# Kernel tuning notes

Measured on AMD Instinct MI355X. Metric: run time of the kernel, lower is better.

The kernel has to match this reference:

```python
import jax, jax.numpy as jnp
import numpy as np

# ---- fixed constants from stft2hcfp.__init__ ----
FS = 16000.0; FR = 2.0; FC = 27.5; TC = 1.0 / 4487.0; NPO = 48
N = int(FS / FR)                      # 8000 FFT length
HALF_N = int(round(N / 2))            # 4000
SQRT_N = float(np.sqrt(N))
HIGH_FREQ_IDX = int(round(1.0 / TC / FR) + 1)   # 2245
HIGH_QUEF_IDX = int(round(FS / FC)) + 1         # 583
CUT_Q = int(round(FS * TC))           # 4  (cepstrum cutoff)
TOTAL_BINS = 4 * 88                   # 352 log-freq bins
NUM_HARMONIC = 5

def _central_freqs():
    stop = 1.0 / TC
    nest = int(np.ceil(np.log2(stop / FC)) * NPO)
    cf = []
    for i in range(nest):
        c = FC * 2.0 ** (float(i) / NPO)
        if c < stop:
            cf.append(c)
        else:
            break
    return cf

CF = _central_freqs()   # 353 central frequencies
NEST = len(CF)

def _freq_matrix():
    # triangular log-frequency filterbank over linear freq axis
    f = (FS * np.linspace(0, 0.5, HALF_N, endpoint=True))[:HIGH_FREQ_IDX]
    W = np.zeros((NEST - 1, len(f)), np.float32)
    for i in range(1, NEST - 1):
        l = int(round(CF[i - 1] / FR)); r = int(round(CF[i + 1] / FR) + 1)
        if l >= r - 1:
            W[i, l] = 1.0
        else:
            for j in range(l, r):
                if CF[i - 1] < f[j] < CF[i]:
                    W[i, j] = (f[j] - CF[i - 1]) / (CF[i] - CF[i - 1])
                elif CF[i] < f[j] < CF[i + 1]:
                    W[i, j] = (CF[i + 1] - f[j]) / (CF[i + 1] - CF[i])
    return W

def _quef_matrix():
    q = np.arange(HIGH_QUEF_IDX) / FS + 1e-6
    fq = 1.0 / q
    W = np.zeros((NEST - 1, len(fq)), np.float32)
    for i in range(1, NEST - 1):
        for j in range(int(round(FS / CF[i + 1])), int(round(FS / CF[i - 1]) + 1)):
            if j >= len(fq):
                continue
            if CF[i - 1] < fq[j] < CF[i]:
                W[i, j] = (fq[j] - CF[i - 1]) / (CF[i] - CF[i - 1])
            elif CF[i] < fq[j] < CF[i + 1]:
                W[i, j] = (CF[i + 1] - fq[j]) / (CF[i + 1] - CF[i])
    return W

# harmonic shift indices: closest central freq to (k+1)*27.5 Hz, k=0..5
HIDS = [int(np.argmin(np.abs(np.asarray(CF) - (k + 1) * FC))) for k in range(NUM_HARMONIC + 1)]


def _nonlinear(x, g, cutoff):
    # relu + pow(g), then zero first/last `cutoff` rows along axis 1.
    # safe pow: grad is 0 where x<=0 (matches relu-masked torch behavior, no inf at 0)
    y = jnp.where(x > 0, jnp.where(x > 0, x, 1.0) ** g, 0.0)
    y = y.at[:, :cutoff].set(0.0).at[:, -cutoff:].set(0.0)
    return y


def setup_inputs() -> dict:
    key = jax.random.key(0)
    dx = jax.random.uniform(key, (8, 512, N), dtype=jnp.float32)  # [B, T, 8000] spectrogram
    return {
        "dx": dx,
        "W_freq": jnp.asarray(_freq_matrix()),   # [352, 2245]
        "W_quef": jnp.asarray(_quef_matrix()),   # [352, 583]
    }


def reference(dx, W_freq, W_quef):
    tfr0 = jnp.swapaxes(dx, 1, 2)                       # [B, F=8000, T]
    # CFP layer 1: real part of FFT over freq axis -> cepstrum, nonlinear g=0.6
    ceps = jnp.fft.fft(tfr0, axis=1).real / SQRT_N      # [B, 8000, T]
    ceps = _nonlinear(ceps, 0.6, CUT_Q)
    # log-frequency mappings (banded triangular filterbanks)
    tfr0h = tfr0[:, :HIGH_FREQ_IDX]                      # [B, 2245, T]
    cepsh = ceps[:, :HIGH_QUEF_IDX]                      # [B, 583, T]
    tfrL0 = jnp.einsum('kf,bft->bkt', W_freq, tfr0h)     # [B, 352, T]
    tfrLQ = jnp.einsum('kq,bqt->bkt', W_quef, cepsh)     # [B, 352, T]
    # harmonic stacking: shift down (spectral) / shift up (cepstral)
    har_s = [jnp.pad(tfrL0[:, h:TOTAL_BINS], ((0, 0), (0, h), (0, 0))) for h in HIDS]
    har_c = [jnp.pad(tfrLQ[:, :TOTAL_BINS - h], ((0, 0), (h, 0), (0, 0))) for h in HIDS]
    piece = jnp.concatenate([jnp.stack(har_s, axis=1), jnp.stack(har_c, axis=1)], axis=1)
    return jnp.swapaxes(piece, 2, 3)                     # [B, 12, T, 352]
```

## Files before the change

kernel.cpp:

```cpp
#include <hip/hip_runtime.h>
#include <hip/hip_bf16.h>
#include <limits.h>

typedef __attribute__((ext_vector_type(8))) short short8;
typedef __attribute__((ext_vector_type(4))) float f32x4;
typedef __attribute__((ext_vector_type(16))) float f32x16;

#define NN 8000
#define NCOL 4096
#define KBINS 352
#define QPAD 640
#define QH 160
#define BN 128
#define KC 4
#define NTILE 64
#define KSTEP 16
#define CUTQ 4
#define T_ 512
#define WFB 64
#define WQB 20

#define GLL16(g, l) __builtin_amdgcn_global_load_lds( \
    (const __attribute__((address_space(1))) unsigned int*)(g), \
    (__attribute__((address_space(3))) unsigned int*)(l), 16, 0, 0)

static __device__ __forceinline__ ushort bfc(float f){
  __hip_bfloat16 h = __float2bfloat16(f);
  return *reinterpret_cast<ushort*>(&h);
}
static __device__ __forceinline__ float b2f(ushort u){
  unsigned v = ((unsigned)u) << 16; float f; __builtin_memcpy(&f, &v, 4); return f;
}

__global__ void gen_cos_k(ushort* __restrict__ cosg, int HQI){
  int n = blockIdx.x*256 + threadIdx.x;
  int q = blockIdx.y;
  float v = 0.f;
  if (q < HQI){
    int m = (q*n) % NN;
    v = cosf((float)m * 7.8539816339744831e-4f);
  }
  int kt = n >> 6, s8 = (n >> 3) & 7, e = n & 7;
  cosg[(size_t)kt*(QPAD*64) + (size_t)q*64 + (((s8 ^ (q & 7)) << 3) | e)] = bfc(v);
}

#define PADI(j) ((j) + ((j) >> 5))
__global__ __launch_bounds__(512) void fold_k(const float* __restrict__ dx,
                                              ushort* __restrict__ xf){
  __shared__ float sbuf[4232];
  int row = blockIdx.x;
  int t = threadIdx.x;
  const float* rp = dx + (size_t)row*NN;
  {
    int j0 = t*8;
    f32x4 v0 = *(const f32x4*)(rp + 3896 + j0);
    f32x4 v1 = *(const f32x4*)(rp + 3896 + j0 + 4);
    #pragma unroll
    for (int e=0;e<4;e++) sbuf[PADI(j0+e)] = v0[e];
    #pragma unroll
    for (int e=0;e<4;e++) sbuf[PADI(j0+4+e)] = v1[e];
    if (t == 0){
      #pragma unroll
      for (int e=0;e<8;e++) sbuf[PADI(4096+e)] = rp[7992+e];
    }
  }
  __syncthreads();

  int n0 = t*8;
  f32x4 p0 = *(const f32x4*)(rp + n0);
  f32x4 p1 = *(const f32x4*)(rp + n0 + 4);
  float pr[8] = {p0[0],p0[1],p0[2],p0[3],p1[0],p1[1],p1[2],p1[3]};
  short8 o;
  #pragma unroll
  for (int e=0;e<8;e++){
    int n = n0 + e;
    float v;
    if (n == 0)          v = pr[0];
    else if (n < 4000)   v = pr[e] + sbuf[PADI(4104 - n)];
    else if (n == 4000)  v = pr[e];
    else                 v = 0.f;
    o[e] = (short)bfc(v);
  }
  int kt = n0 >> 6, s8 = (n0 >> 3) & 7;
  *(short8*)(&xf[((size_t)kt*NCOL + row)*64 + ((s8 ^ (row & 7)) << 3)]) = o;
}

__global__ void bp_k(const float* __restrict__ Wf, const float* __restrict__ Wq,
                     int HFI, int HQI, int* __restrict__ fLo, int* __restrict__ qLo,
                     float* __restrict__ WfT, float* __restrict__ WqT){
  __shared__ int slo, shi;
  int r = blockIdx.x;
  bool isF = (blockIdx.y == 0);
  const float* W = isF ? Wf : Wq;
  int width = isF ? HFI : HQI;
  int bw    = isF ? WFB : WQB;
  float* WT = isF ? WfT : WqT;
  int* Lo   = isF ? fLo : qLo;
  if (threadIdx.x==0){ slo = INT_MAX; shi = -1; }
  __syncthreads();
  int mylo = INT_MAX, myhi = -1;
  for (int c = threadIdx.x; c < width; c += 256){
    if (W[(size_t)r*width + c] != 0.f){ if (c < mylo) mylo = c; if (c > myhi) myhi = c; }
  }
  atomicMin(&slo, mylo); atomicMax(&shi, myhi);
  __syncthreads();
  int l = (shi < 0) ? 0 : slo, h = (shi < 0) ? 0 : shi + 1;
  if (threadIdx.x==0) Lo[r] = l;
  for (int j = threadIdx.x; j < bw; j += 256){
    float v = 0.f;
    if (l + j < h) v = W[(size_t)r*width + l + j];
    WT[(size_t)j*KBINS + r] = v;
  }
}

__global__ __launch_bounds__(256, 2) void gemm_k(const ushort* __restrict__ xf,
                                                 const ushort* __restrict__ cosg,
                                                 ushort* __restrict__ part){
  __shared__ ushort As[2][QH*64];
  __shared__ ushort Bs[2][BN*64];
  int tid = threadIdx.x;
  int nb = blockIdx.x, qh = blockIdx.y, kc = blockIdx.z;
  int lane = tid & 63, wn = tid >> 6;
  int l31 = lane & 31, lh = lane >> 5;
  int kt0 = kc*KSTEP, ktE = kt0 + KSTEP;

  const ushort* ag0 = cosg + (size_t)qh*(QH*64) + tid*8;
  const ushort* bg0 = xf + (size_t)nb*(BN*64) + tid*8;

  #define STAGE(kt_, buf_) { \
    const ushort* ag_ = ag0 + (size_t)(kt_)*(QPAD*64); \
    _Pragma("unroll") \
    for (int i_=0;i_<5;i_++) GLL16(ag_ + i_*2048, &As[buf_][tid*8 + i_*2048]); \
    const ushort* bg_ = bg0 + (size_t)(kt_)*(NCOL*64); \
    _Pragma("unroll") \
    for (int i_=0;i_<4;i_++) GLL16(bg_ + i_*2048, &Bs[buf_][tid*8 + i_*2048]); }

  f32x16 acc[5];
  #pragma unroll
  for (int a=0;a<5;a++) acc[a] = (f32x16)0.f;

  STAGE(kt0, 0);

  int cur = 0;
  for (int kt = kt0; kt < ktE; ++kt){
    bool stg = (kt + 1 < ktE);
    if (stg){
      STAGE(kt+1, cur^1);
      asm volatile("s_waitcnt vmcnt(9)" ::: "memory");
    } else {
      asm volatile("s_waitcnt vmcnt(0)" ::: "memory");
    }
    __builtin_amdgcn_s_barrier();
    __builtin_amdgcn_sched_barrier(0);
    const ushort* Ac = &As[cur][0];
    const ushort* Bc = &Bs[cur][0];
    #pragma unroll
    for (int p=0;p<4;p++){
      int brow = wn*32 + l31;
      short8 dfr = *(const short8*)(Bc + brow*64 + ((((p<<1)|lh) ^ (brow & 7)) << 3));
      short8 cfr[5];
      #pragma unroll
      for (int a=0;a<5;a++){
        int arow = a*32 + l31;
        cfr[a] = *(const short8*)(Ac + arow*64 + ((((p<<1)|lh) ^ (arow & 7)) << 3));
      }
      __builtin_amdgcn_s_setprio(1);
      #pragma unroll
      for (int a=0;a<5;a++)
        acc[a] = __builtin_amdgcn_mfma_f32_32x32x16_bf16(dfr, cfr[a], acc[a], 0,0,0);
      __builtin_amdgcn_s_setprio(0);
    }
    __builtin_amdgcn_sched_barrier(0);
    __builtin_amdgcn_s_barrier();
    __builtin_amdgcn_sched_barrier(0);
    cur ^= 1;
  }

  ushort* pb = part + (size_t)kc*NCOL*QPAD;
  #pragma unroll
  for (int a=0;a<5;a++){
    int q = qh*QH + a*32 + l31;
    int colb = nb*BN + wn*32 + 4*lh;
    #pragma unroll
    for (int r=0;r<16;r++){
      int col = colb + (r&3) + 8*(r>>2);
      pb[(size_t)col*QPAD + q] = bfc(acc[a][r]);
    }
  }
}

__global__ __launch_bounds__(384) void fuse_k(const float* __restrict__ dx,
        const ushort* __restrict__ part,
        const float* __restrict__ WfT, const float* __restrict__ WqT,
        const int* __restrict__ fLo, const int* __restrict__ qLo,
        float* __restrict__ out, int HFI, int HQI){
  __shared__ float xr[2368];
  __shared__ float yq[QPAD];
  __shared__ float tl0[KBINS];
  __shared__ float tlq[KBINS];
  int col = blockIdx.x;
  int b = col >> 9, t = col & 511;
  int tid = threadIdx.x;
  const float invs = 0.011180339887498949f;

  for (int f = tid; f < 2368; f += 384) xr[f] = (f < HFI) ? dx[(size_t)col*NN + f] : 0.f;
  const ushort* pc = part + (size_t)col*QPAD;
  for (int q = tid; q < QPAD; q += 384){
    float y = 0.f;
    if (q < HQI){
      float s = 0.f;
      #pragma unroll
      for (int kc=0; kc<KC; kc++) s += b2f(pc[(size_t)kc*NCOL*QPAD + q]);
      s *= invs;
      if (q >= CUTQ && s > 0.f) y = powf(s, 0.6f);
    }
    yq[q] = y;
  }
  __syncthreads();

  if (tid < KBINS){
    int k = tid;
    int lo = fLo[k];
    float aF = 0.f;
    #pragma unroll
    for (int j=0;j<WFB;j++) aF += WfT[j*KBINS + k] * xr[lo + j];
    int ql = qLo[k];
    float aQ = 0.f;
    #pragma unroll
    for (int j=0;j<WQB;j++) aQ += WqT[j*KBINS + k] * yq[ql + j];
    tl0[k] = aF; tlq[k] = aQ;
  }
  __syncthreads();

  const int hids[6] = {0,48,76,96,111,124};
  for (int u = tid; u < 12*KBINS; u += 384){
    int j = u / KBINS;
    int k = u - j*KBINS;
    int h = hids[(j < 6) ? j : j - 6];
    float v;
    if (j < 6) v = (k + h < KBINS) ? tl0[k + h] : 0.f;
    else       v = (k >= h)        ? tlq[k - h] : 0.f;
    out[(((size_t)b*12 + j)*T_ + t)*KBINS + k] = v;
  }
}

extern "C" void kernel_launch(void* const* d_in, const int* in_sizes, int n_in,
                              void* d_out, int out_size, void* d_ws, size_t ws_size,
                              hipStream_t stream){
  const float* dx = (const float*)d_in[0];
  const float* Wf = (const float*)d_in[1];
  const float* Wq = (const float*)d_in[2];
  int HFI = in_sizes[1] / KBINS;
  int HQI = in_sizes[2] / KBINS;
  float* out = (float*)d_out;
  char* ws = (char*)d_ws;

  ushort* cosg = (ushort*)ws;
  size_t off = (size_t)NTILE*QPAD*64*2;
  ushort* xf = (ushort*)(ws + off); off += (size_t)NTILE*NCOL*64*2;
  ushort* part = (ushort*)(ws + off); off += (size_t)KC*NCOL*QPAD*2;
  int* fLo = (int*)(ws+off); off += KBINS*4;
  int* qLo = (int*)(ws+off); off += KBINS*4;
  float* WfT = (float*)(ws+off); off += (size_t)WFB*KBINS*4;
  float* WqT = (float*)(ws+off); off += (size_t)WQB*KBINS*4;
  (void)n_in; (void)out_size; (void)ws_size;

  gen_cos_k<<<dim3(16, QPAD), 256, 0, stream>>>(cosg, HQI);
  fold_k<<<NCOL, 512, 0, stream>>>(dx, xf);
  bp_k<<<dim3(KBINS, 2), 256, 0, stream>>>(Wf, Wq, HFI, HQI, fLo, qLo, WfT, WqT);
  gemm_k<<<dim3(NCOL/BN, QPAD/QH, KC), 256, 0, stream>>>(xf, cosg, part);
  fuse_k<<<NCOL, 384, 0, stream>>>(dx, part, WfT, WqT, fLo, qLo, out, HFI, HQI);
}
```

Baseline: 129.4 us.

## Enlarge GEMM tiles with eight-wave blocks, deepen split-K, merge prep kernels

The cosine GEMM tile grows to 320x256 with 512 threads. The eight waves are arranged 2x4, and each wave computes a 5x2 set of 32x32 MFMA accumulators, so every LDS fragment is reused more. Split-K goes from 4 to 8 chunks, which keeps the block count at one per CU but doubles the bf16 partial-sum traffic that fuse_k has to reduce. The three setup kernels (cos table, fold, band extraction) are merged into one launch that branches on block index, removing launch gaps. The LDS footprint roughly doubles, so only one block fits per CU, and the block barrier now runs once per p sub-step rather than once per k-tile.

```diff
diff --git a/kernel.cpp b/kernel.cpp
--- a/kernel.cpp
+++ b/kernel.cpp
@@ -10,15 +10,16 @@
 #define NCOL 4096
 #define KBINS 352
 #define QPAD 640
-#define QH 160
-#define BN 128
-#define KC 4
+#define QH 320
+#define BN 256
+#define KC 8
 #define NTILE 64
-#define KSTEP 16
+#define KSTEP 8
 #define CUTQ 4
 #define T_ 512
 #define WFB 64
 #define WQB 20
+#define NGC 2560
 
 #define GLL16(g, l) __builtin_amdgcn_global_load_lds( \
     (const __attribute__((address_space(1))) unsigned int*)(g), \
@@ -32,95 +33,102 @@
   unsigned v = ((unsigned)u) << 16; float f; __builtin_memcpy(&f, &v, 4); return f;
 }
 
-__global__ void gen_cos_k(ushort* __restrict__ cosg, int HQI){
-  int n = blockIdx.x*256 + threadIdx.x;
-  int q = blockIdx.y;
-  float v = 0.f;
-  if (q < HQI){
-    int m = (q*n) % NN;
-    v = cosf((float)m * 7.8539816339744831e-4f);
-  }
-  int kt = n >> 6, s8 = (n >> 3) & 7, e = n & 7;
-  cosg[(size_t)kt*(QPAD*64) + (size_t)q*64 + (((s8 ^ (q & 7)) << 3) | e)] = bfc(v);
-}
-
 #define PADI(j) ((j) + ((j) >> 5))
-__global__ __launch_bounds__(512) void fold_k(const float* __restrict__ dx,
-                                              ushort* __restrict__ xf){
+
+__global__ __launch_bounds__(512) void prep_k(const float* __restrict__ dx,
+        ushort* __restrict__ xf, ushort* __restrict__ cosg,
+        const float* __restrict__ Wf, const float* __restrict__ Wq,
+        int HFI, int HQI, int* __restrict__ fLo, int* __restrict__ qLo,
+        float* __restrict__ WfT, float* __restrict__ WqT){
   __shared__ float sbuf[4232];
-  int row = blockIdx.x;
+  __shared__ int slo, shi;
+  int bid = blockIdx.x;
   int t = threadIdx.x;
-  const float* rp = dx + (size_t)row*NN;
-  {
-    int j0 = t*8;
-    f32x4 v0 = *(const f32x4*)(rp + 3896 + j0);
-    f32x4 v1 = *(const f32x4*)(rp + 3896 + j0 + 4);
-    #pragma unroll
-    for (int e=0;e<4;e++) sbuf[PADI(j0+e)] = v0[e];
-    #pragma unroll
-    for (int e=0;e<4;e++) sbuf[PADI(j0+4+e)] = v1[e];
-    if (t == 0){
-      #pragma unroll
-      for (int e=0;e<8;e++) sbuf[PADI(4096+e)] = rp[7992+e];
-    }
-  }
-  __syncthreads();
-
-  int n0 = t*8;
-  f32x4 p0 = *(const f32x4*)(rp + n0);
-  f32x4 p1 = *(const f32x4*)(rp + n0 + 4);
-  float pr[8] = {p0[0],p0[1],p0[2],p0[3],p1[0],p1[1],p1[2],p1[3]};
-  short8 o;
-  #pragma unroll
-  for (int e=0;e<8;e++){
-    int n = n0 + e;
-    float v;
-    if (n == 0)          v = pr[0];
-    else if (n < 4000)   v = pr[e] + sbuf[PADI(4104 - n)];
-    else if (n == 4000)  v = pr[e];
-    else                 v = 0.f;
-    o[e] = (short)bfc(v);
-  }
-  int kt = n0 >> 6, s8 = (n0 >> 3) & 7;
-  *(short8*)(&xf[((size_t)kt*NCOL + row)*64 + ((s8 ^ (row & 7)) << 3)]) = o;
-}
-
-__global__ void bp_k(const float* __restrict__ Wf, const float* __restrict__ Wq,
-                     int HFI, int HQI, int* __restrict__ fLo, int* __restrict__ qLo,
-                     float* __restrict__ WfT, float* __restrict__ WqT){
-  __shared__ int slo, shi;
-  int r = blockIdx.x;
-  bool isF = (blockIdx.y == 0);
-  const float* W = isF ? Wf : Wq;
-  int width = isF ? HFI : HQI;
-  int bw    = isF ? WFB : WQB;
-  float* WT = isF ? WfT : WqT;
-  int* Lo   = isF ? fLo : qLo;
-  if (threadIdx.x==0){ slo = INT_MAX; shi = -1; }
-  __syncthreads();
-  int mylo = INT_MAX, myhi = -1;
-  for (int c = threadIdx.x; c < width; c += 256){
-    if (W[(size_t)r*width + c] != 0.f){ if (c < mylo) mylo = c; if (c > myhi) myhi = c; }
-  }
-  atomicMin(&slo, mylo); atomicMax(&shi, myhi);
-  __syncthreads();
-  int l = (shi < 0) ? 0 : slo, h = (shi < 0) ? 0 : shi + 1;
-  if (threadIdx.x==0) Lo[r] = l;
-  for (int j = threadIdx.x; j < bw; j += 256){
-    float v = 0.f;
-    if (l + j < h) v = W[(size_t)r*width + l + j];
-    WT[(size_t)j*KBINS + r] = v;
-  }
-}
-
-__global__ __launch_bounds__(256, 2) void gemm_k(const ushort* __restrict__ xf,
+
+  if (bid < NCOL){
+    int row = bid;
+    const float* rp = dx + (size_t)row*NN;
+    {
+      int j0 = t*8;
+      f32x4 v0 = *(const f32x4*)(rp + 3896 + j0);
+      f32x4 v1 = *(const f32x4*)(rp + 3896 + j0 + 4);
+      #pragma unroll
+      for (int e=0;e<4;e++) sbuf[PADI(j0+e)] = v0[e];
+      #pragma unroll
+      for (int e=0;e<4;e++) sbuf[PADI(j0+4+e)] = v1[e];
+      if (t == 0){
+        #pragma unroll
+        for (int e=0;e<8;e++) sbuf[PADI(4096+e)] = rp[7992+e];
+      }
+    }
+    __syncthreads();
+    int n0 = t*8;
+    f32x4 p0 = *(const f32x4*)(rp + n0);
+    f32x4 p1 = *(const f32x4*)(rp + n0 + 4);
+    float pr[8] = {p0[0],p0[1],p0[2],p0[3],p1[0],p1[1],p1[2],p1[3]};
+    short8 o;
+    #pragma unroll
+    for (int e=0;e<8;e++){
+      int n = n0 + e;
+      float v;
+      if (n == 0)          v = pr[0];
+      else if (n < 4000)   v = pr[e] + sbuf[PADI(4104 - n)];
+      else if (n == 4000)  v = pr[e];
+      else                 v = 0.f;
+      o[e] = (short)bfc(v);
+    }
+    int kt = n0 >> 6, s8 = (n0 >> 3) & 7;
+    *(short8*)(&xf[((size_t)kt*NCOL + row)*64 + ((s8 ^ (row & 7)) << 3)]) = o;
+  } else if (bid < NCOL + NGC){
+    int base = (bid - NCOL) * 1024;
+    #pragma unroll
+    for (int u2=0;u2<2;u2++){
+      int id = base + u2*512 + t;
+      int q = id >> 12, n = id & 4095;
+      float v = 0.f;
+      if (q < HQI){
+        int m = (q*n) % NN;
+        v = cosf((float)m * 7.8539816339744831e-4f);
+      }
+      int kt = n >> 6, s8 = (n >> 3) & 7, e = n & 7;
+      cosg[(size_t)kt*(QPAD*64) + (size_t)q*64 + (((s8 ^ (q & 7)) << 3) | e)] = bfc(v);
+    }
+  } else {
+    int u = bid - NCOL - NGC;
+    int r = u >> 1;
+    bool isF = (u & 1) == 0;
+    const float* W = isF ? Wf : Wq;
+    int width = isF ? HFI : HQI;
+    int bw    = isF ? WFB : WQB;
+    float* WT = isF ? WfT : WqT;
+    int* Lo   = isF ? fLo : qLo;
+    if (t==0){ slo = INT_MAX; shi = -1; }
+    __syncthreads();
+    int mylo = INT_MAX, myhi = -1;
+    for (int c = t; c < width; c += 512){
+      if (W[(size_t)r*width + c] != 0.f){ if (c < mylo) mylo = c; if (c > myhi) myhi = c; }
+    }
+    atomicMin(&slo, mylo); atomicMax(&shi, myhi);
+    __syncthreads();
+    int l = (shi < 0) ? 0 : slo, h = (shi < 0) ? 0 : shi + 1;
+    if (t==0) Lo[r] = l;
+    for (int j = t; j < bw; j += 512){
+      float v = 0.f;
+      if (l + j < h) v = W[(size_t)r*width + l + j];
+      WT[(size_t)j*KBINS + r] = v;
+    }
+  }
+}
+
+__global__ __launch_bounds__(512, 2) void gemm_k(const ushort* __restrict__ xf,
                                                  const ushort* __restrict__ cosg,
                                                  ushort* __restrict__ part){
   __shared__ ushort As[2][QH*64];
   __shared__ ushort Bs[2][BN*64];
   int tid = threadIdx.x;
   int nb = blockIdx.x, qh = blockIdx.y, kc = blockIdx.z;
-  int lane = tid & 63, wn = tid >> 6;
+  int lane = tid & 63, widx = tid >> 6;
+  int wm = widx & 1, wn = widx >> 1;
   int l31 = lane & 31, lh = lane >> 5;
   int kt0 = kc*KSTEP, ktE = kt0 + KSTEP;
 
@@ -130,21 +138,20 @@
   #define STAGE(kt_, buf_) { \
     const ushort* ag_ = ag0 + (size_t)(kt_)*(QPAD*64); \
     _Pragma("unroll") \
-    for (int i_=0;i_<5;i_++) GLL16(ag_ + i_*2048, &As[buf_][tid*8 + i_*2048]); \
+    for (int i_=0;i_<5;i_++) GLL16(ag_ + i_*4096, &As[buf_][tid*8 + i_*4096]); \
     const ushort* bg_ = bg0 + (size_t)(kt_)*(NCOL*64); \
     _Pragma("unroll") \
-    for (int i_=0;i_<4;i_++) GLL16(bg_ + i_*2048, &Bs[buf_][tid*8 + i_*2048]); }
-
-  f32x16 acc[5];
+    for (int i_=0;i_<4;i_++) GLL16(bg_ + i_*4096, &Bs[buf_][tid*8 + i_*4096]); }
+
+  f32x16 acc[5][2];
   #pragma unroll
-  for (int a=0;a<5;a++) acc[a] = (f32x16)0.f;
+  for (int a=0;a<5;a++){ acc[a][0] = (f32x16)0.f; acc[a][1] = (f32x16)0.f; }
 
   STAGE(kt0, 0);
 
   int cur = 0;
   for (int kt = kt0; kt < ktE; ++kt){
-    bool stg = (kt + 1 < ktE);
-    if (stg){
+    if (kt + 1 < ktE){
       STAGE(kt+1, cur^1);
       asm volatile("s_waitcnt vmcnt(9)" ::: "memory");
     } else {
@@ -156,35 +163,44 @@
     const ushort* Bc = &Bs[cur][0];
     #pragma unroll
     for (int p=0;p<4;p++){
-      int brow = wn*32 + l31;
-      short8 dfr = *(const short8*)(Bc + brow*64 + ((((p<<1)|lh) ^ (brow & 7)) << 3));
+      short8 dfr[2];
+      #pragma unroll
+      for (int c=0;c<2;c++){
+        int row = wn*64 + c*32 + l31;
+        dfr[c] = *(const short8*)(Bc + row*64 + ((((p<<1)|lh) ^ (row & 7)) << 3));
+      }
       short8 cfr[5];
       #pragma unroll
       for (int a=0;a<5;a++){
-        int arow = a*32 + l31;
-        cfr[a] = *(const short8*)(Ac + arow*64 + ((((p<<1)|lh) ^ (arow & 7)) << 3));
+        int row = wm*160 + a*32 + l31;
+        cfr[a] = *(const short8*)(Ac + row*64 + ((((p<<1)|lh) ^ (row & 7)) << 3));
       }
       __builtin_amdgcn_s_setprio(1);
       #pragma unroll
-      for (int a=0;a<5;a++)
-        acc[a] = __builtin_amdgcn_mfma_f32_32x32x16_bf16(dfr, cfr[a], acc[a], 0,0,0);
+      for (int a=0;a<5;a++){
+        acc[a][0] = __builtin_amdgcn_mfma_f32_32x32x16_bf16(dfr[0], cfr[a], acc[a][0], 0,0,0);
+        acc[a][1] = __builtin_amdgcn_mfma_f32_32x32x16_bf16(dfr[1], cfr[a], acc[a][1], 0,0,0);
+      }
       __builtin_amdgcn_s_setprio(0);
-    }
-    __builtin_amdgcn_sched_barrier(0);
-    __builtin_amdgcn_s_barrier();
-    __builtin_amdgcn_sched_barrier(0);
+      __builtin_amdgcn_sched_barrier(0);
+      __builtin_amdgcn_s_barrier();
+      __builtin_amdgcn_sched_barrier(0);
+    }
     cur ^= 1;
   }
 
   ushort* pb = part + (size_t)kc*NCOL*QPAD;
   #pragma unroll
   for (int a=0;a<5;a++){
-    int q = qh*QH + a*32 + l31;
-    int colb = nb*BN + wn*32 + 4*lh;
-    #pragma unroll
-    for (int r=0;r<16;r++){
-      int col = colb + (r&3) + 8*(r>>2);
-      pb[(size_t)col*QPAD + q] = bfc(acc[a][r]);
+    int q = qh*QH + wm*160 + a*32 + l31;
+    #pragma unroll
+    for (int c=0;c<2;c++){
+      int colb = nb*BN + wn*64 + c*32 + 4*lh;
+      #pragma unroll
+      for (int r=0;r<16;r++){
+        int col = colb + (r&3) + 8*(r>>2);
+        pb[(size_t)col*QPAD + q] = bfc(acc[a][c][r]);
+      }
     }
   }
 }
@@ -265,9 +281,8 @@
   float* WqT = (float*)(ws+off); off += (size_t)WQB*KBINS*4;
   (void)n_in; (void)out_size; (void)ws_size;
 
-  gen_cos_k<<<dim3(16, QPAD), 256, 0, stream>>>(cosg, HQI);
-  fold_k<<<NCOL, 512, 0, stream>>>(dx, xf);
-  bp_k<<<dim3(KBINS, 2), 256, 0, stream>>>(Wf, Wq, HFI, HQI, fLo, qLo, WfT, WqT);
-  gemm_k<<<dim3(NCOL/BN, QPAD/QH, KC), 256, 0, stream>>>(xf, cosg, part);
+  prep_k<<<NCOL + NGC + 2*KBINS, 512, 0, stream>>>(dx, xf, cosg, Wf, Wq,
+                                                   HFI, HQI, fLo, qLo, WfT, WqT);
+  gemm_k<<<dim3(NCOL/BN, QPAD/QH, KC), 512, 0, stream>>>(xf, cosg, part);
   fuse_k<<<NCOL, 384, 0, stream>>>(dx, part, WfT, WqT, fLo, qLo, out, HFI, HQI);
 }
```

Measured after the change: 128.5 us. No clear change (-0.7%).
